# Performance work log

Hardware: AMD Instinct MI355X
Metric: run time of the kernel (lower is better)

## Reference

```python
import jax, jax.numpy as jnp
import numpy as np

B, L, TQ, D, H, S = 4, 64, 8, 768, 12, 2000
E = D // H
EPS = 1e-5


def _ln(x, g, b):
    m = jnp.mean(x, axis=-1, keepdims=True)
    v = jnp.mean(jnp.square(x - m), axis=-1, keepdims=True)
    return (x - m) * jax.lax.rsqrt(v + EPS) * g + b


def setup_inputs() -> dict:
    key = jax.random.key(0)
    ks = jax.random.split(key, 8)
    w = 0.02
    return {
        "target_tokens": jax.random.normal(ks[0], (B, L, TQ, D), jnp.float32),
        "key_bank": jax.random.normal(ks[1], (S, D), jnp.float32),
        "value_bank": jax.random.normal(ks[2], (S, D), jnp.float32),
        "bank_mask": jnp.ones((S,), jnp.int32),
        "Wq": jax.random.normal(ks[3], (D, D), jnp.float32) * w,
        "bq": jnp.zeros((D,), jnp.float32),
        "Wk": jax.random.normal(ks[4], (D, D), jnp.float32) * w,
        "bk": jnp.zeros((D,), jnp.float32),
        "Wv": jax.random.normal(ks[5], (D, D), jnp.float32) * w,
        "bv": jnp.zeros((D,), jnp.float32),
        "Wo": jax.random.normal(ks[6], (D, D), jnp.float32) * w,
        "bo": jnp.zeros((D,), jnp.float32),
        "g_q": jnp.ones((D,), jnp.float32),
        "beta_q": jnp.zeros((D,), jnp.float32),
        "g_kv": jnp.ones((D,), jnp.float32),
        "beta_kv": jnp.zeros((D,), jnp.float32),
    }


def reference(target_tokens, key_bank, value_bank, bank_mask,
              Wq, bq, Wk, bk, Wv, bv, Wo, bo,
              g_q, beta_q, g_kv, beta_kv):
    scale = 1.0 / np.sqrt(E)
    # LayerNorms
    Q_in = _ln(target_tokens, g_q, beta_q)            # (B,L,Tq,D)
    K_in = _ln(key_bank, g_kv, beta_kv)               # (S,D)
    V_in = _ln(value_bank, g_kv, beta_kv)             # (S,D)
    # Projections (torch Linear: x @ W.T + b)
    Q = (jnp.einsum('bltd,ed->blte', Q_in, Wq) + bq).reshape(B, L, TQ, H, E)
    K = (jnp.einsum('sd,ed->se', K_in, Wk) + bk).reshape(S, H, E)
    V = (jnp.einsum('sd,ed->se', V_in, Wv) + bv).reshape(S, H, E)
    # Scores over the bank (bank is shared across batch)
    scores = jnp.einsum('blthe,she->bhlts', Q, K) * scale  # (B,H,L,Tq,S)
    mask = bank_mask[None, None, None, None, :] != 0
    scores = jnp.where(mask, scores, -jnp.inf)
    A = jax.nn.softmax(scores, axis=-1)
    out = jnp.einsum('bhlts,she->blthe', A, V)             # (B,L,Tq,H,E)
    out_pooled = out.mean(axis=2).reshape(B, L, H * E)     # pool='mean' over Tq
    y = jnp.einsum('bld,ed->ble', out_pooled, Wo) + bo     # (B,L,D)
    return y
```

## Files before the change

### kernel.cpp

```cpp
#include <hip/hip_runtime.h>
#include <stdint.h>

typedef unsigned short u16;
typedef float f32x4 __attribute__((ext_vector_type(4)));
typedef __bf16 bf16x8 __attribute__((ext_vector_type(8)));

#define DDIM 768
#define NHEAD 12
#define EDIM 64
#define SREAL 2000
#define SPAD 2048
#define NQ 2048
#define NSPLIT 4

__device__ __forceinline__ u16 f2bf(float f) {
    unsigned u = __float_as_uint(f);
    return (u16)((u + 0x7fffu + ((u >> 16) & 1u)) >> 16);
}
__device__ __forceinline__ float bf2f(u16 v) {
    return __uint_as_float(((unsigned)v) << 16);
}

__device__ __forceinline__ void async16(const void* g, void* l) {
    __builtin_amdgcn_global_load_lds(
        (const __attribute__((address_space(1))) void*)(const void*)g,
        (__attribute__((address_space(3))) void*)l, 16, 0, 0);
}

__global__ __launch_bounds__(256) void prep_kernel(
    const float* __restrict__ Wq, const float* __restrict__ Wk, const float* __restrict__ Wv,
    const float* __restrict__ Wo,
    u16* __restrict__ Wqb, u16* __restrict__ Wkb, u16* __restrict__ Wvb, u16* __restrict__ Wob,
    const float* __restrict__ tgt, const float* __restrict__ keyb, const float* __restrict__ valb,
    const float* __restrict__ g_q, const float* __restrict__ b_q,
    const float* __restrict__ g_kv, const float* __restrict__ b_kv,
    u16* __restrict__ lnQ, u16* __restrict__ lnK, u16* __restrict__ lnV)
{
    int bx = blockIdx.x;
    if (bx < 2304) {
        int g = bx * 256 + threadIdx.x;
        const float* src; u16* dst; int idx; float sc = 1.f;
        if (g < 147456)      { src = Wq; dst = Wqb; idx = g; sc = 0.125f; }
        else if (g < 294912) { src = Wk; dst = Wkb; idx = g - 147456; }
        else if (g < 442368) { src = Wv; dst = Wvb; idx = g - 294912; }
        else                 { src = Wo; dst = Wob; idx = g - 442368; }
        f32x4 a = ((const f32x4*)src)[idx];
        ushort4 o;
        o.x = f2bf(a[0] * sc); o.y = f2bf(a[1] * sc);
        o.z = f2bf(a[2] * sc); o.w = f2bf(a[3] * sc);
        ((ushort4*)dst)[idx] = o;
        return;
    }
    int row = (bx - 2304) * 4 + (threadIdx.x >> 6);
    int l = threadIdx.x & 63;
    const float* src = nullptr; const float* gg; const float* bb; u16* dst;
    bool zero = false;
    if (row < 2048) {
        src = tgt + (size_t)row * DDIM; gg = g_q; bb = b_q; dst = lnQ + (size_t)row * DDIM;
    } else if (row < 4096) {
        int r = row - 2048; gg = g_kv; bb = b_kv; dst = lnK + (size_t)r * DDIM;
        if (r < SREAL) src = keyb + (size_t)r * DDIM; else zero = true;
    } else {
        int r = row - 4096; gg = g_kv; bb = b_kv; dst = lnV + (size_t)r * DDIM;
        if (r < SREAL) src = valb + (size_t)r * DDIM; else zero = true;
    }
    if (zero) {
        ushort4 z; z.x = 0; z.y = 0; z.z = 0; z.w = 0;
#pragma unroll
        for (int i = 0; i < 3; i++) ((ushort4*)dst)[l + 64 * i] = z;
        return;
    }
    f32x4 a[3];
#pragma unroll
    for (int i = 0; i < 3; i++) a[i] = ((const f32x4*)src)[l + 64 * i];
    float s = 0.f;
#pragma unroll
    for (int i = 0; i < 3; i++) { s += a[i][0] + a[i][1] + a[i][2] + a[i][3]; }
#pragma unroll
    for (int m = 1; m < 64; m <<= 1) s += __shfl_xor(s, m, 64);
    float mean = s * (1.f / 768.f);
    float v = 0.f;
#pragma unroll
    for (int i = 0; i < 3; i++)
#pragma unroll
        for (int j = 0; j < 4; j++) { float d = a[i][j] - mean; v += d * d; }
#pragma unroll
    for (int m = 1; m < 64; m <<= 1) v += __shfl_xor(v, m, 64);
    float rstd = rsqrtf(v * (1.f / 768.f) + 1e-5f);
#pragma unroll
    for (int i = 0; i < 3; i++) {
        f32x4 g4 = ((const f32x4*)gg)[l + 64 * i];
        f32x4 b4 = ((const f32x4*)bb)[l + 64 * i];
        ushort4 o;
        o.x = f2bf((a[i][0] - mean) * rstd * g4[0] + b4[0]);
        o.y = f2bf((a[i][1] - mean) * rstd * g4[1] + b4[1]);
        o.z = f2bf((a[i][2] - mean) * rstd * g4[2] + b4[2]);
        o.w = f2bf((a[i][3] - mean) * rstd * g4[3] + b4[3]);
        ((ushort4*)dst)[l + 64 * i] = o;
    }
}

__global__ __launch_bounds__(256) void proj_kernel(
    const u16* __restrict__ lnQ, const u16* __restrict__ lnK, const u16* __restrict__ lnV,
    const u16* __restrict__ Wqb, const u16* __restrict__ Wkb, const u16* __restrict__ Wvb,
    const float* __restrict__ bq, const float* __restrict__ bk, const float* __restrict__ bv,
    u16* __restrict__ Qm, u16* __restrict__ Km, u16* __restrict__ VmT)
{
    __shared__ u16 Ash[2][128 * 64];
    __shared__ u16 Bsh[2][64 * 64];
    const u16* A; const u16* W; const float* bias; float bscale; int z = blockIdx.z;
    if (z == 0)      { A = lnQ; W = Wqb; bias = bq; bscale = 0.125f; }
    else if (z == 1) { A = lnK; W = Wkb; bias = bk; bscale = 1.f; }
    else             { A = lnV; W = Wvb; bias = bv; bscale = 1.f; }
    int n0 = blockIdx.x * 64, m0 = blockIdx.y * 128;
    int t = threadIdx.x, l = t & 63, quad = l >> 4, c16 = l & 15;
    int w = t >> 6;

    f32x4 acc[2][4];
    f32x4 zz = {0.f, 0.f, 0.f, 0.f};
#pragma unroll
    for (int mi = 0; mi < 2; mi++)
#pragma unroll
        for (int ni = 0; ni < 4; ni++) acc[mi][ni] = zz;

#pragma unroll
    for (int i = 0; i < 4; i++) {
        int ch = i * 256 + t;
        int r = ch >> 3, pc = ch & 7, jc = pc ^ (r & 7);
        async16(A + (size_t)(m0 + r) * DDIM + jc * 8, (char*)Ash[0] + ch * 16);
    }
#pragma unroll
    for (int i = 0; i < 2; i++) {
        int ch = i * 256 + t;
        int r = ch >> 3, pc = ch & 7, jc = pc ^ (r & 7);
        async16(W + (size_t)(n0 + r) * DDIM + jc * 8, (char*)Bsh[0] + ch * 16);
    }
    for (int kt = 0; kt < 12; kt++) {
        int cur = kt & 1;
        __syncthreads();
        if (kt < 11) {
            int k0 = (kt + 1) * 64;
#pragma unroll
            for (int i = 0; i < 4; i++) {
                int ch = i * 256 + t;
                int r = ch >> 3, pc = ch & 7, jc = pc ^ (r & 7);
                async16(A + (size_t)(m0 + r) * DDIM + k0 + jc * 8, (char*)Ash[cur ^ 1] + ch * 16);
            }
#pragma unroll
            for (int i = 0; i < 2; i++) {
                int ch = i * 256 + t;
                int r = ch >> 3, pc = ch & 7, jc = pc ^ (r & 7);
                async16(W + (size_t)(n0 + r) * DDIM + k0 + jc * 8, (char*)Bsh[cur ^ 1] + ch * 16);
            }
        }
#pragma unroll
        for (int kk = 0; kk < 2; kk++) {
            bf16x8 a[2], b[4];
#pragma unroll
            for (int mi = 0; mi < 2; mi++) {
                int row = w * 32 + mi * 16 + c16;
                int p = (kk * 4 + quad) ^ (row & 7);
                a[mi] = *(const bf16x8*)(Ash[cur] + row * 64 + p * 8);
            }
#pragma unroll
            for (int ni = 0; ni < 4; ni++) {
                int row = ni * 16 + c16;
                int p = (kk * 4 + quad) ^ (row & 7);
                b[ni] = *(const bf16x8*)(Bsh[cur] + row * 64 + p * 8);
            }
#pragma unroll
            for (int mi = 0; mi < 2; mi++)
#pragma unroll
                for (int ni = 0; ni < 4; ni++)
                    acc[mi][ni] = __builtin_amdgcn_mfma_f32_16x16x32_bf16(a[mi], b[ni], acc[mi][ni], 0, 0, 0);
        }
        __syncthreads();
    }
    if (z < 2) {
        u16* out = (z == 0) ? Qm : Km;
        int Mact = (z == 0) ? NQ : SREAL;
#pragma unroll
        for (int mi = 0; mi < 2; mi++)
#pragma unroll
            for (int ni = 0; ni < 4; ni++) {
                int n = n0 + ni * 16 + c16;
                float bval = bias[n] * bscale;
#pragma unroll
                for (int r = 0; r < 4; r++) {
                    int m = m0 + w * 32 + mi * 16 + quad * 4 + r;
                    float val = (m < Mact) ? (acc[mi][ni][r] + bval) : 0.f;
                    out[(size_t)m * DDIM + n] = f2bf(val);
                }
            }
    } else {
#pragma unroll
        for (int mi = 0; mi < 2; mi++)
#pragma unroll
            for (int ni = 0; ni < 4; ni++) {
                int n = n0 + ni * 16 + c16;
                float bval = bias[n];
                int mbase = m0 + w * 32 + mi * 16 + quad * 4;
                ushort4 o;
                o.x = (mbase + 0 < SREAL) ? f2bf(acc[mi][ni][0] + bval) : (u16)0;
                o.y = (mbase + 1 < SREAL) ? f2bf(acc[mi][ni][1] + bval) : (u16)0;
                o.z = (mbase + 2 < SREAL) ? f2bf(acc[mi][ni][2] + bval) : (u16)0;
                o.w = (mbase + 3 < SREAL) ? f2bf(acc[mi][ni][3] + bval) : (u16)0;
                *(ushort4*)(VmT + (size_t)n * SPAD + mbase) = o;
            }
    }
}

__global__ __launch_bounds__(256, 4) void attn_kernel(
    const u16* __restrict__ Qm, const u16* __restrict__ Km, const u16* __restrict__ VmT,
    const int* __restrict__ bank_mask,
    u16* __restrict__ Opart, float* __restrict__ Lpart)
{
    __shared__ __align__(16) u16 SH[64 * 64 * 3];
    __shared__ float mk[64];
    u16* Ksh = SH;
    u16* Vsh = SH + 4096;
    u16* Psh = SH + 8192;
    int b = blockIdx.x;
    int xcd = b & 7, j = b >> 3;
    int grp = xcd * 6 + (j >> 5);
    int qt = j & 31;
    int sp = grp / NHEAD, h = grp - sp * NHEAD;
    int q0 = qt * 64;
    int t = threadIdx.x, w = t >> 6, l = t & 63, quad = l >> 4, c16 = l & 15;

    bf16x8 qf[2];
#pragma unroll
    for (int kk = 0; kk < 2; kk++) {
        int row = q0 + w * 16 + c16;
        qf[kk] = *(const bf16x8*)(Qm + (size_t)row * DDIM + h * EDIM + kk * 32 + quad * 8);
    }
    bf16x8 ones;
#pragma unroll
    for (int i = 0; i < 8; i++) ones[i] = (__bf16)1.0f;

    f32x4 zz = {0.f, 0.f, 0.f, 0.f};
    f32x4 of[4], ol;
#pragma unroll
    for (int nei = 0; nei < 4; nei++) of[nei] = zz;
    ol = zz;

    for (int sc = 0; sc < 8; sc++) {
        int s0 = sp * 512 + sc * 64;
#pragma unroll
        for (int i = 0; i < 2; i++) {
            int ch = i * 256 + t;
            int r = ch >> 3, pc = ch & 7, jc = pc ^ (r & 7);
            async16(Km + (size_t)(s0 + r) * DDIM + h * EDIM + jc * 8, (char*)Ksh + ch * 16);
        }
#pragma unroll
        for (int i = 0; i < 2; i++) {
            int ch = i * 256 + t;
            int e = ch >> 3, pc = ch & 7, jc = pc ^ (e & 7);
            async16(VmT + (size_t)(h * EDIM + e) * SPAD + s0 + jc * 8, (char*)Vsh + ch * 16);
        }
        if (t < 64) {
            int s = s0 + t;
            mk[t] = (s < SREAL && bank_mask[s] != 0) ? 1.f : 0.f;
        }
        __syncthreads();

        f32x4 sacc[4];
#pragma unroll
        for (int ni = 0; ni < 4; ni++) sacc[ni] = zz;
#pragma unroll
        for (int kk = 0; kk < 2; kk++) {
            bf16x8 kb[4];
#pragma unroll
            for (int ni = 0; ni < 4; ni++) {
                int row = ni * 16 + c16;
                int p = (kk * 4 + quad) ^ (row & 7);
                kb[ni] = *(const bf16x8*)(Ksh + row * 64 + p * 8);
            }
#pragma unroll
            for (int ni = 0; ni < 4; ni++)
                sacc[ni] = __builtin_amdgcn_mfma_f32_16x16x32_bf16(qf[kk], kb[ni], sacc[ni], 0, 0, 0);
        }
        float m01[4];
#pragma unroll
        for (int ni = 0; ni < 4; ni++) m01[ni] = mk[ni * 16 + c16];
#pragma unroll
        for (int ni = 0; ni < 4; ni++)
#pragma unroll
            for (int r = 0; r < 4; r++)
                sacc[ni][r] = __expf(sacc[ni][r]) * m01[ni];

#pragma unroll
        for (int ni = 0; ni < 4; ni++)
#pragma unroll
            for (int r = 0; r < 4; r++) {
                int row = w * 16 + quad * 4 + r;
                int col = ni * 16 + c16;
                int p = (col >> 3) ^ (row & 7);
                Psh[row * 64 + p * 8 + (col & 7)] = f2bf(sacc[ni][r]);
            }

#pragma unroll
        for (int kk = 0; kk < 2; kk++) {
            bf16x8 pa, vb[4];
            {
                int row = w * 16 + c16;
                int p = (kk * 4 + quad) ^ (row & 7);
                pa = *(const bf16x8*)(Psh + row * 64 + p * 8);
            }
#pragma unroll
            for (int nei = 0; nei < 4; nei++) {
                int e = nei * 16 + c16;
                int p = (kk * 4 + quad) ^ (e & 7);
                vb[nei] = *(const bf16x8*)(Vsh + e * 64 + p * 8);
            }
#pragma unroll
            for (int nei = 0; nei < 4; nei++)
                of[nei] = __builtin_amdgcn_mfma_f32_16x16x32_bf16(pa, vb[nei], of[nei], 0, 0, 0);
            ol = __builtin_amdgcn_mfma_f32_16x16x32_bf16(pa, ones, ol, 0, 0, 0);
        }
        __syncthreads();
    }

    float* Ost = (float*)SH + w * (16 * 68);
#pragma unroll
    for (int nei = 0; nei < 4; nei++)
#pragma unroll
        for (int r = 0; r < 4; r++)
            Ost[(quad * 4 + r) * 68 + nei * 16 + c16] = of[nei][r];
    int qq = l >> 2, cc = (l & 3) ^ (qq & 3);
    int base = grp * 32 + qt;
    uint4 packed[2];
    u16* pk = (u16*)packed;
#pragma unroll
    for (int jj = 0; jj < 4; jj++) {
        f32x4 v = *(const f32x4*)(Ost + qq * 68 + cc * 16 + jj * 4);
        pk[jj * 4 + 0] = f2bf(v[0]); pk[jj * 4 + 1] = f2bf(v[1]);
        pk[jj * 4 + 2] = f2bf(v[2]); pk[jj * 4 + 3] = f2bf(v[3]);
    }
    {
        u16* dst = Opart + (size_t)base * 4096 + (w * 16 + qq) * 64 + cc * 16;
        *(uint4*)dst = packed[0];
        *(uint4*)(dst + 8) = packed[1];
    }
    if (c16 == 0) {
#pragma unroll
        for (int r = 0; r < 4; r++) {
            int rin = w * 16 + quad * 4 + r;
            Lpart[(size_t)base * 64 + rin] = ol[r];
        }
    }
}

__global__ __launch_bounds__(256) void combine_kernel(
    const u16* __restrict__ Opart, const float* __restrict__ Lpart,
    u16* __restrict__ pooledb)
{
    int gi = blockIdx.x * 4 + (threadIdx.x >> 6);
    int e = threadIdx.x & 63;
    int lq = gi / NHEAD, h = gi - lq * NHEAD;
    float acc = 0.f;
#pragma unroll
    for (int row = 0; row < 8; row++) {
        int qrow = lq * 8 + row;
        int qt = qrow >> 6, rin = qrow & 63;
        float Ls = 0.f, val = 0.f;
#pragma unroll
        for (int sp = 0; sp < NSPLIT; sp++) {
            int base = (sp * NHEAD + h) * 32 + qt;
            Ls += Lpart[(size_t)base * 64 + rin];
            val += bf2f(Opart[(size_t)base * 4096 + rin * 64 + e]);
        }
        acc += val / Ls;
    }
    pooledb[(size_t)lq * DDIM + h * EDIM + e] = f2bf(acc * 0.125f);
}

__global__ __launch_bounds__(256) void wo_kernel(
    const u16* __restrict__ pb, const u16* __restrict__ Wob,
    const float* __restrict__ bo, float* __restrict__ y)
{
    __shared__ u16 Ash[64 * 128];
    __shared__ u16 Bsh[64 * 128];
    int m0 = blockIdx.x * 64, n0 = blockIdx.y * 64;
    int t = threadIdx.x, w = t >> 6, l = t & 63, quad = l >> 4, c16 = l & 15;

    f32x4 acc[4];
    f32x4 zz = {0.f, 0.f, 0.f, 0.f};
#pragma unroll
    for (int ni = 0; ni < 4; ni++) acc[ni] = zz;

    for (int kt = 0; kt < 6; kt++) {
        int k0 = kt * 128;
#pragma unroll
        for (int i = 0; i < 4; i++) {
            int ch = i * 256 + t;
            int r = ch >> 4, pc = ch & 15, jc = pc ^ (r & 15);
            async16(pb + (size_t)(m0 + r) * DDIM + k0 + jc * 8, (char*)Ash + ch * 16);
            async16(Wob + (size_t)(n0 + r) * DDIM + k0 + jc * 8, (char*)Bsh + ch * 16);
        }
        __syncthreads();
#pragma unroll
        for (int kk = 0; kk < 4; kk++) {
            int p = (kk * 4 + quad) ^ c16;
            bf16x8 a = *(const bf16x8*)(Ash + (w * 16 + c16) * 128 + p * 8);
            bf16x8 b[4];
#pragma unroll
            for (int ni = 0; ni < 4; ni++)
                b[ni] = *(const bf16x8*)(Bsh + (ni * 16 + c16) * 128 + p * 8);
#pragma unroll
            for (int ni = 0; ni < 4; ni++)
                acc[ni] = __builtin_amdgcn_mfma_f32_16x16x32_bf16(a, b[ni], acc[ni], 0, 0, 0);
        }
        __syncthreads();
    }
#pragma unroll
    for (int ni = 0; ni < 4; ni++) {
        int n = n0 + ni * 16 + c16;
        float bval = bo[n];
#pragma unroll
        for (int r = 0; r < 4; r++) {
            int m = m0 + w * 16 + quad * 4 + r;
            y[(size_t)m * DDIM + n] = acc[ni][r] + bval;
        }
    }
}

extern "C" void kernel_launch(void* const* d_in, const int* in_sizes, int n_in,
                              void* d_out, int out_size, void* d_ws, size_t ws_size,
                              hipStream_t stream)
{
    const float* tgt     = (const float*)d_in[0];
    const float* keyb    = (const float*)d_in[1];
    const float* valb    = (const float*)d_in[2];
    const int*   mask    = (const int*)d_in[3];
    const float* Wq      = (const float*)d_in[4];
    const float* bq      = (const float*)d_in[5];
    const float* Wk      = (const float*)d_in[6];
    const float* bk      = (const float*)d_in[7];
    const float* Wv      = (const float*)d_in[8];
    const float* bv      = (const float*)d_in[9];
    const float* Wo      = (const float*)d_in[10];
    const float* bo      = (const float*)d_in[11];
    const float* g_q     = (const float*)d_in[12];
    const float* beta_q  = (const float*)d_in[13];
    const float* g_kv    = (const float*)d_in[14];
    const float* beta_kv = (const float*)d_in[15];
    float* y = (float*)d_out;

    char* ws = (char*)d_ws;
    u16* Qm  = (u16*)(ws + 0);
    u16* Km  = (u16*)(ws + 3145728);
    u16* VmT = (u16*)(ws + 6291456);
    u16* Wob = (u16*)(ws + 9437184);
    u16* lnQ = (u16*)(ws + 10616832);
    u16* lnK = (u16*)(ws + 13762560);
    u16* lnV = (u16*)(ws + 16908288);
    u16* Wqb = (u16*)(ws + 20054016);
    u16* Wkb = (u16*)(ws + 21233664);
    u16* Wvb = (u16*)(ws + 22413312);
    u16*   Opart   = (u16*)(ws + 10616832);
    float* Lpart   = (float*)(ws + 23592960);
    u16*   pooledb = (u16*)(ws + 23986176);

    hipLaunchKernelGGL(prep_kernel, dim3(3840), dim3(256), 0, stream,
                       Wq, Wk, Wv, Wo, Wqb, Wkb, Wvb, Wob,
                       tgt, keyb, valb, g_q, beta_q, g_kv, beta_kv, lnQ, lnK, lnV);
    hipLaunchKernelGGL(proj_kernel, dim3(12, 16, 3), dim3(256), 0, stream,
                       lnQ, lnK, lnV, Wqb, Wkb, Wvb, bq, bk, bv, Qm, Km, VmT);
    hipLaunchKernelGGL(attn_kernel, dim3(1536), dim3(256), 0, stream,
                       Qm, Km, VmT, mask, Opart, Lpart);
    hipLaunchKernelGGL(combine_kernel, dim3(768), dim3(256), 0, stream,
                       Opart, Lpart, pooledb);
    hipLaunchKernelGGL(wo_kernel, dim3(4, 12), dim3(256), 0, stream,
                       pooledb, Wob, bo, y);
}
```

Before: 159.2 us.

## Fuse all stages into one persistent kernel with software grid barriers

Replaces the five separate launches (prep, projection, attention, combine, output projection) with a single persistent kernel of 512 blocks. The blocks loop over each stage's work units and synchronise through an atomic-counter grid barrier kept in the workspace, which is reset by a memset before each launch. The aim is to remove the launch gaps and tail effects between the small kernels. In exchange, attention occupancy drops from 4 to 2 blocks per CU under the new launch bounds, and there is a co-residency assumption plus a spin-timeout barrier that could break if not all 512 blocks are resident.

```diff
diff --git a/kernel.cpp b/kernel.cpp
--- a/kernel.cpp
+++ b/kernel.cpp
@@ -12,6 +12,8 @@
 #define SPAD 2048
 #define NQ 2048
 #define NSPLIT 4
+#define GRID 512
+#define BAR_OFF 25165824
 
 __device__ __forceinline__ u16 f2bf(float f) {
     unsigned u = __float_as_uint(f);
@@ -27,7 +29,28 @@
         (__attribute__((address_space(3))) void*)l, 16, 0, 0);
 }
 
-__global__ __launch_bounds__(256) void prep_kernel(
+__device__ __forceinline__ void grid_barrier(unsigned* bar) {
+    __syncthreads();
+    if (threadIdx.x == 0) {
+        __builtin_amdgcn_fence(__ATOMIC_SEQ_CST, "");
+        unsigned g = __hip_atomic_load(&bar[32], __ATOMIC_RELAXED, __HIP_MEMORY_SCOPE_SYSTEM);
+        unsigned a = __hip_atomic_fetch_add(&bar[0], 1u, __ATOMIC_ACQ_REL, __HIP_MEMORY_SCOPE_SYSTEM);
+        if (a == GRID - 1u) {
+            __hip_atomic_store(&bar[0], 0u, __ATOMIC_RELAXED, __HIP_MEMORY_SCOPE_SYSTEM);
+            __hip_atomic_fetch_add(&bar[32], 1u, __ATOMIC_RELEASE, __HIP_MEMORY_SCOPE_SYSTEM);
+        } else {
+            int tries = 1 << 20;
+            while (__hip_atomic_load(&bar[32], __ATOMIC_RELAXED, __HIP_MEMORY_SCOPE_SYSTEM) == g) {
+                __builtin_amdgcn_s_sleep(2);
+                if (--tries == 0) break;
+            }
+        }
+        __builtin_amdgcn_fence(__ATOMIC_SEQ_CST, "");
+    }
+    __syncthreads();
+}
+
+__device__ __forceinline__ void prep_unit(int bx, int t,
     const float* __restrict__ Wq, const float* __restrict__ Wk, const float* __restrict__ Wv,
     const float* __restrict__ Wo,
     u16* __restrict__ Wqb, u16* __restrict__ Wkb, u16* __restrict__ Wvb, u16* __restrict__ Wob,
@@ -36,9 +59,8 @@
     const float* __restrict__ g_kv, const float* __restrict__ b_kv,
     u16* __restrict__ lnQ, u16* __restrict__ lnK, u16* __restrict__ lnV)
 {
-    int bx = blockIdx.x;
     if (bx < 2304) {
-        int g = bx * 256 + threadIdx.x;
+        int g = bx * 256 + t;
         const float* src; u16* dst; int idx; float sc = 1.f;
         if (g < 147456)      { src = Wq; dst = Wqb; idx = g; sc = 0.125f; }
         else if (g < 294912) { src = Wk; dst = Wkb; idx = g - 147456; }
@@ -51,8 +73,8 @@
         ((ushort4*)dst)[idx] = o;
         return;
     }
-    int row = (bx - 2304) * 4 + (threadIdx.x >> 6);
-    int l = threadIdx.x & 63;
+    int row = (bx - 2304) * 4 + (t >> 6);
+    int l = t & 63;
     const float* src = nullptr; const float* gg; const float* bb; u16* dst;
     bool zero = false;
     if (row < 2048) {
@@ -100,20 +122,19 @@
     }
 }
 
-__global__ __launch_bounds__(256) void proj_kernel(
+__device__ __forceinline__ void proj_tile(int z, int m0, int n0, int t,
     const u16* __restrict__ lnQ, const u16* __restrict__ lnK, const u16* __restrict__ lnV,
     const u16* __restrict__ Wqb, const u16* __restrict__ Wkb, const u16* __restrict__ Wvb,
     const float* __restrict__ bq, const float* __restrict__ bk, const float* __restrict__ bv,
-    u16* __restrict__ Qm, u16* __restrict__ Km, u16* __restrict__ VmT)
+    u16* __restrict__ Qm, u16* __restrict__ Km, u16* __restrict__ VmT, char* SMEMC)
 {
-    __shared__ u16 Ash[2][128 * 64];
-    __shared__ u16 Bsh[2][64 * 64];
-    const u16* A; const u16* W; const float* bias; float bscale; int z = blockIdx.z;
+    u16* Ash0 = (u16*)SMEMC;
+    u16* Bsh0 = (u16*)(SMEMC + 32768);
+    const u16* A; const u16* W; const float* bias; float bscale;
     if (z == 0)      { A = lnQ; W = Wqb; bias = bq; bscale = 0.125f; }
     else if (z == 1) { A = lnK; W = Wkb; bias = bk; bscale = 1.f; }
     else             { A = lnV; W = Wvb; bias = bv; bscale = 1.f; }
-    int n0 = blockIdx.x * 64, m0 = blockIdx.y * 128;
-    int t = threadIdx.x, l = t & 63, quad = l >> 4, c16 = l & 15;
+    int l = t & 63, quad = l >> 4, c16 = l & 15;
     int w = t >> 6;
 
     f32x4 acc[2][4];
@@ -127,13 +148,13 @@
     for (int i = 0; i < 4; i++) {
         int ch = i * 256 + t;
         int r = ch >> 3, pc = ch & 7, jc = pc ^ (r & 7);
-        async16(A + (size_t)(m0 + r) * DDIM + jc * 8, (char*)Ash[0] + ch * 16);
+        async16(A + (size_t)(m0 + r) * DDIM + jc * 8, (char*)Ash0 + ch * 16);
     }
 #pragma unroll
     for (int i = 0; i < 2; i++) {
         int ch = i * 256 + t;
         int r = ch >> 3, pc = ch & 7, jc = pc ^ (r & 7);
-        async16(W + (size_t)(n0 + r) * DDIM + jc * 8, (char*)Bsh[0] + ch * 16);
+        async16(W + (size_t)(n0 + r) * DDIM + jc * 8, (char*)Bsh0 + ch * 16);
     }
     for (int kt = 0; kt < 12; kt++) {
         int cur = kt & 1;
@@ -144,13 +165,15 @@
             for (int i = 0; i < 4; i++) {
                 int ch = i * 256 + t;
                 int r = ch >> 3, pc = ch & 7, jc = pc ^ (r & 7);
-                async16(A + (size_t)(m0 + r) * DDIM + k0 + jc * 8, (char*)Ash[cur ^ 1] + ch * 16);
+                async16(A + (size_t)(m0 + r) * DDIM + k0 + jc * 8,
+                        (char*)(Ash0 + (cur ^ 1) * 8192) + ch * 16);
             }
 #pragma unroll
             for (int i = 0; i < 2; i++) {
                 int ch = i * 256 + t;
                 int r = ch >> 3, pc = ch & 7, jc = pc ^ (r & 7);
-                async16(W + (size_t)(n0 + r) * DDIM + k0 + jc * 8, (char*)Bsh[cur ^ 1] + ch * 16);
+                async16(W + (size_t)(n0 + r) * DDIM + k0 + jc * 8,
+                        (char*)(Bsh0 + (cur ^ 1) * 4096) + ch * 16);
             }
         }
 #pragma unroll
@@ -160,13 +183,13 @@
             for (int mi = 0; mi < 2; mi++) {
                 int row = w * 32 + mi * 16 + c16;
                 int p = (kk * 4 + quad) ^ (row & 7);
-                a[mi] = *(const bf16x8*)(Ash[cur] + row * 64 + p * 8);
+                a[mi] = *(const bf16x8*)(Ash0 + cur * 8192 + row * 64 + p * 8);
             }
 #pragma unroll
             for (int ni = 0; ni < 4; ni++) {
                 int row = ni * 16 + c16;
                 int p = (kk * 4 + quad) ^ (row & 7);
-                b[ni] = *(const bf16x8*)(Bsh[cur] + row * 64 + p * 8);
+                b[ni] = *(const bf16x8*)(Bsh0 + cur * 4096 + row * 64 + p * 8);
             }
 #pragma unroll
             for (int mi = 0; mi < 2; mi++)
@@ -210,23 +233,19 @@
     }
 }
 
-__global__ __launch_bounds__(256, 4) void attn_kernel(
+__device__ __forceinline__ void attn_tile(int grp, int qt, int t,
     const u16* __restrict__ Qm, const u16* __restrict__ Km, const u16* __restrict__ VmT,
     const int* __restrict__ bank_mask,
-    u16* __restrict__ Opart, float* __restrict__ Lpart)
+    u16* __restrict__ Opart, float* __restrict__ Lpart, char* SMEMC)
 {
-    __shared__ __align__(16) u16 SH[64 * 64 * 3];
-    __shared__ float mk[64];
+    u16* SH = (u16*)SMEMC;
+    float* mk = (float*)(SMEMC + 24576);
     u16* Ksh = SH;
     u16* Vsh = SH + 4096;
     u16* Psh = SH + 8192;
-    int b = blockIdx.x;
-    int xcd = b & 7, j = b >> 3;
-    int grp = xcd * 6 + (j >> 5);
-    int qt = j & 31;
     int sp = grp / NHEAD, h = grp - sp * NHEAD;
     int q0 = qt * 64;
-    int t = threadIdx.x, w = t >> 6, l = t & 63, quad = l >> 4, c16 = l & 15;
+    int w = t >> 6, l = t & 63, quad = l >> 4, c16 = l & 15;
 
     bf16x8 qf[2];
 #pragma unroll
@@ -349,40 +368,16 @@
             Lpart[(size_t)base * 64 + rin] = ol[r];
         }
     }
-}
-
-__global__ __launch_bounds__(256) void combine_kernel(
-    const u16* __restrict__ Opart, const float* __restrict__ Lpart,
-    u16* __restrict__ pooledb)
+    __syncthreads();
+}
+
+__device__ __forceinline__ void wo_tile(int m0, int n0, int t,
+    const u16* __restrict__ pb, const u16* __restrict__ Wob,
+    const float* __restrict__ bo, float* __restrict__ y, char* SMEMC)
 {
-    int gi = blockIdx.x * 4 + (threadIdx.x >> 6);
-    int e = threadIdx.x & 63;
-    int lq = gi / NHEAD, h = gi - lq * NHEAD;
-    float acc = 0.f;
-#pragma unroll
-    for (int row = 0; row < 8; row++) {
-        int qrow = lq * 8 + row;
-        int qt = qrow >> 6, rin = qrow & 63;
-        float Ls = 0.f, val = 0.f;
-#pragma unroll
-        for (int sp = 0; sp < NSPLIT; sp++) {
-            int base = (sp * NHEAD + h) * 32 + qt;
-            Ls += Lpart[(size_t)base * 64 + rin];
-            val += bf2f(Opart[(size_t)base * 4096 + rin * 64 + e]);
-        }
-        acc += val / Ls;
-    }
-    pooledb[(size_t)lq * DDIM + h * EDIM + e] = f2bf(acc * 0.125f);
-}
-
-__global__ __launch_bounds__(256) void wo_kernel(
-    const u16* __restrict__ pb, const u16* __restrict__ Wob,
-    const float* __restrict__ bo, float* __restrict__ y)
-{
-    __shared__ u16 Ash[64 * 128];
-    __shared__ u16 Bsh[64 * 128];
-    int m0 = blockIdx.x * 64, n0 = blockIdx.y * 64;
-    int t = threadIdx.x, w = t >> 6, l = t & 63, quad = l >> 4, c16 = l & 15;
+    u16* Ash = (u16*)SMEMC;
+    u16* Bsh = (u16*)(SMEMC + 16384);
+    int w = t >> 6, l = t & 63, quad = l >> 4, c16 = l & 15;
 
     f32x4 acc[4];
     f32x4 zz = {0.f, 0.f, 0.f, 0.f};
@@ -422,6 +417,89 @@
             int m = m0 + w * 16 + quad * 4 + r;
             y[(size_t)m * DDIM + n] = acc[ni][r] + bval;
         }
+    }
+}
+
+__global__ __launch_bounds__(256, 2) void mega_kernel(
+    const float* __restrict__ tgt, const float* __restrict__ keyb, const float* __restrict__ valb,
+    const int* __restrict__ bank_mask,
+    const float* __restrict__ Wq, const float* __restrict__ bq,
+    const float* __restrict__ Wk, const float* __restrict__ bk,
+    const float* __restrict__ Wv, const float* __restrict__ bv,
+    const float* __restrict__ Wo, const float* __restrict__ bo,
+    const float* __restrict__ g_q, const float* __restrict__ beta_q,
+    const float* __restrict__ g_kv, const float* __restrict__ beta_kv,
+    char* ws, float* y)
+{
+    __shared__ __align__(16) char SMEM[49152];
+    int bid = blockIdx.x, t = threadIdx.x;
+
+    u16* Qm  = (u16*)(ws + 0);
+    u16* Km  = (u16*)(ws + 3145728);
+    u16* VmT = (u16*)(ws + 6291456);
+    u16* Wob = (u16*)(ws + 9437184);
+    u16* lnQ = (u16*)(ws + 10616832);
+    u16* lnK = (u16*)(ws + 13762560);
+    u16* lnV = (u16*)(ws + 16908288);
+    u16* Wqb = (u16*)(ws + 20054016);
+    u16* Wkb = (u16*)(ws + 21233664);
+    u16* Wvb = (u16*)(ws + 22413312);
+    u16*   Opart   = (u16*)(ws + 10616832);
+    float* Lpart   = (float*)(ws + 23592960);
+    u16*   pooledb = (u16*)(ws + 23986176);
+    unsigned* bar  = (unsigned*)(ws + BAR_OFF);
+
+    for (int u = bid; u < 3840; u += GRID)
+        prep_unit(u, t, Wq, Wk, Wv, Wo, Wqb, Wkb, Wvb, Wob,
+                  tgt, keyb, valb, g_q, beta_q, g_kv, beta_kv, lnQ, lnK, lnV);
+    grid_barrier(bar);
+
+    for (int tl = bid; tl < 576; tl += GRID) {
+        int z = tl / 192, rem = tl - z * 192;
+        int m0 = (rem / 12) * 128;
+        int n0 = (rem - (rem / 12) * 12) * 64;
+        proj_tile(z, m0, n0, t, lnQ, lnK, lnV, Wqb, Wkb, Wvb, bq, bk, bv,
+                  Qm, Km, VmT, SMEM);
+        __syncthreads();
+    }
+    grid_barrier(bar);
+
+#pragma unroll
+    for (int it = 0; it < 3; it++) {
+        int T = bid + it * GRID;
+        int xcd = T & 7, j = T >> 3;
+        int grp = xcd * 6 + (j >> 5);
+        int qt = j & 31;
+        attn_tile(grp, qt, t, Qm, Km, VmT, bank_mask, Opart, Lpart, SMEM);
+    }
+    grid_barrier(bar);
+
+    for (int unit = bid; unit < 768; unit += GRID) {
+        int gi = unit * 4 + (t >> 6);
+        int e = t & 63;
+        int lq = gi / NHEAD, h = gi - lq * NHEAD;
+        float acc = 0.f;
+#pragma unroll
+        for (int row = 0; row < 8; row++) {
+            int qrow = lq * 8 + row;
+            int qt = qrow >> 6, rin = qrow & 63;
+            float Ls = 0.f, val = 0.f;
+#pragma unroll
+            for (int sp = 0; sp < NSPLIT; sp++) {
+                int base = (sp * NHEAD + h) * 32 + qt;
+                Ls += Lpart[(size_t)base * 64 + rin];
+                val += bf2f(Opart[(size_t)base * 4096 + rin * 64 + e]);
+            }
+            acc += val / Ls;
+        }
+        pooledb[(size_t)lq * DDIM + h * EDIM + e] = f2bf(acc * 0.125f);
+    }
+    grid_barrier(bar);
+
+    if (bid < 48) {
+        int m0 = (bid & 3) * 64;
+        int n0 = (bid >> 2) * 64;
+        wo_tile(m0, n0, t, pooledb, Wob, bo, y, SMEM);
     }
 }
 
@@ -446,31 +524,11 @@
     const float* g_kv    = (const float*)d_in[14];
     const float* beta_kv = (const float*)d_in[15];
     float* y = (float*)d_out;
-
     char* ws = (char*)d_ws;
-    u16* Qm  = (u16*)(ws + 0);
-    u16* Km  = (u16*)(ws + 3145728);
-    u16* VmT = (u16*)(ws + 6291456);
-    u16* Wob = (u16*)(ws + 9437184);
-    u16* lnQ = (u16*)(ws + 10616832);
-    u16* lnK = (u16*)(ws + 13762560);
-    u16* lnV = (u16*)(ws + 16908288);
-    u16* Wqb = (u16*)(ws + 20054016);
-    u16* Wkb = (u16*)(ws + 21233664);
-    u16* Wvb = (u16*)(ws + 22413312);
-    u16*   Opart   = (u16*)(ws + 10616832);
-    float* Lpart   = (float*)(ws + 23592960);
-    u16*   pooledb = (u16*)(ws + 23986176);
-
-    hipLaunchKernelGGL(prep_kernel, dim3(3840), dim3(256), 0, stream,
-                       Wq, Wk, Wv, Wo, Wqb, Wkb, Wvb, Wob,
-                       tgt, keyb, valb, g_q, beta_q, g_kv, beta_kv, lnQ, lnK, lnV);
-    hipLaunchKernelGGL(proj_kernel, dim3(12, 16, 3), dim3(256), 0, stream,
-                       lnQ, lnK, lnV, Wqb, Wkb, Wvb, bq, bk, bv, Qm, Km, VmT);
-    hipLaunchKernelGGL(attn_kernel, dim3(1536), dim3(256), 0, stream,
-                       Qm, Km, VmT, mask, Opart, Lpart);
-    hipLaunchKernelGGL(combine_kernel, dim3(768), dim3(256), 0, stream,
-                       Opart, Lpart, pooledb);
-    hipLaunchKernelGGL(wo_kernel, dim3(4, 12), dim3(256), 0, stream,
-                       pooledb, Wob, bo, y);
-}
+
+    hipMemsetAsync(ws + BAR_OFF, 0, 256, stream);
+
+    hipLaunchKernelGGL(mega_kernel, dim3(GRID), dim3(256), 0, stream,
+                       tgt, keyb, valb, mask, Wq, bq, Wk, bk, Wv, bv, Wo, bo,
+                       g_q, beta_q, g_kv, beta_kv, ws, y);
+}
```

Result: slower. 301.5 us (+89.3%).

## Double-buffer K/V tiles in attention and precompute bank mask bits in registers

Applied to the files above, without the earlier changes.

The attention kernel now keeps two K/V tile buffers in LDS and issues the async loads for the next 64-row bank chunk before computing on the current one. This overlaps global-to-LDS traffic with MFMA work and removes one barrier per iteration. The per-chunk mask load into shared memory is replaced by a 32-bit register bitmask built once at kernel start. A trailing __syncthreads in the projection GEMM loop is also dropped. The larger LDS footprint can lower occupancy, and dropping the GEMM barrier relies on its existing buffering to stay race-free.

```diff
diff --git a/kernel.cpp b/kernel.cpp
--- a/kernel.cpp
+++ b/kernel.cpp
@@ -174,7 +174,6 @@
                 for (int ni = 0; ni < 4; ni++)
                     acc[mi][ni] = __builtin_amdgcn_mfma_f32_16x16x32_bf16(a[mi], b[ni], acc[mi][ni], 0, 0, 0);
         }
-        __syncthreads();
     }
     if (z < 2) {
         u16* out = (z == 0) ? Qm : Km;
@@ -215,11 +214,8 @@
     const int* __restrict__ bank_mask,
     u16* __restrict__ Opart, float* __restrict__ Lpart)
 {
-    __shared__ __align__(16) u16 SH[64 * 64 * 3];
-    __shared__ float mk[64];
-    u16* Ksh = SH;
-    u16* Vsh = SH + 4096;
-    u16* Psh = SH + 8192;
+    __shared__ __align__(16) u16 SH[64 * 64 * 5];
+    u16* Psh = SH + 16384;
     int b = blockIdx.x;
     int xcd = b & 7, j = b >> 3;
     int grp = xcd * 6 + (j >> 5);
@@ -238,31 +234,59 @@
 #pragma unroll
     for (int i = 0; i < 8; i++) ones[i] = (__bf16)1.0f;
 
+    unsigned mbits = 0;
+#pragma unroll
+    for (int sc = 0; sc < 8; sc++)
+#pragma unroll
+        for (int ni = 0; ni < 4; ni++) {
+            int s = sp * 512 + sc * 64 + ni * 16 + c16;
+            int ok = (s < SREAL) ? bank_mask[s] : 0;
+            mbits |= (ok != 0 ? 1u : 0u) << (sc * 4 + ni);
+        }
+
     f32x4 zz = {0.f, 0.f, 0.f, 0.f};
     f32x4 of[4], ol;
 #pragma unroll
     for (int nei = 0; nei < 4; nei++) of[nei] = zz;
     ol = zz;
 
-    for (int sc = 0; sc < 8; sc++) {
-        int s0 = sp * 512 + sc * 64;
+    {
+        int s0 = sp * 512;
 #pragma unroll
         for (int i = 0; i < 2; i++) {
             int ch = i * 256 + t;
             int r = ch >> 3, pc = ch & 7, jc = pc ^ (r & 7);
-            async16(Km + (size_t)(s0 + r) * DDIM + h * EDIM + jc * 8, (char*)Ksh + ch * 16);
+            async16(Km + (size_t)(s0 + r) * DDIM + h * EDIM + jc * 8, (char*)SH + ch * 16);
         }
 #pragma unroll
         for (int i = 0; i < 2; i++) {
             int ch = i * 256 + t;
             int e = ch >> 3, pc = ch & 7, jc = pc ^ (e & 7);
-            async16(VmT + (size_t)(h * EDIM + e) * SPAD + s0 + jc * 8, (char*)Vsh + ch * 16);
-        }
-        if (t < 64) {
-            int s = s0 + t;
-            mk[t] = (s < SREAL && bank_mask[s] != 0) ? 1.f : 0.f;
-        }
+            async16(VmT + (size_t)(h * EDIM + e) * SPAD + s0 + jc * 8, (char*)(SH + 8192) + ch * 16);
+        }
+    }
+
+    for (int sc = 0; sc < 8; sc++) {
         __syncthreads();
+        if (sc < 7) {
+            int s0 = sp * 512 + (sc + 1) * 64;
+            u16* Kd = SH + ((sc + 1) & 1) * 4096;
+            u16* Vd = SH + 8192 + ((sc + 1) & 1) * 4096;
+#pragma unroll
+            for (int i = 0; i < 2; i++) {
+                int ch = i * 256 + t;
+                int r = ch >> 3, pc = ch & 7, jc = pc ^ (r & 7);
+                async16(Km + (size_t)(s0 + r) * DDIM + h * EDIM + jc * 8, (char*)Kd + ch * 16);
+            }
+#pragma unroll
+            for (int i = 0; i < 2; i++) {
+                int ch = i * 256 + t;
+                int e = ch >> 3, pc = ch & 7, jc = pc ^ (e & 7);
+                async16(VmT + (size_t)(h * EDIM + e) * SPAD + s0 + jc * 8, (char*)Vd + ch * 16);
+            }
+        }
+        const u16* Kc = SH + (sc & 1) * 4096;
+        const u16* Vc = SH + 8192 + (sc & 1) * 4096;
 
         f32x4 sacc[4];
 #pragma unroll
@@ -274,20 +298,19 @@
             for (int ni = 0; ni < 4; ni++) {
                 int row = ni * 16 + c16;
                 int p = (kk * 4 + quad) ^ (row & 7);
-                kb[ni] = *(const bf16x8*)(Ksh + row * 64 + p * 8);
+                kb[ni] = *(const bf16x8*)(Kc + row * 64 + p * 8);
             }
 #pragma unroll
             for (int ni = 0; ni < 4; ni++)
                 sacc[ni] = __builtin_amdgcn_mfma_f32_16x16x32_bf16(qf[kk], kb[ni], sacc[ni], 0, 0, 0);
         }
-        float m01[4];
-#pragma unroll
-        for (int ni = 0; ni < 4; ni++) m01[ni] = mk[ni * 16 + c16];
-#pragma unroll
-        for (int ni = 0; ni < 4; ni++)
+#pragma unroll
+        for (int ni = 0; ni < 4; ni++) {
+            float m01 = (float)((mbits >> (sc * 4 + ni)) & 1u);
 #pragma unroll
             for (int r = 0; r < 4; r++)
-                sacc[ni][r] = __expf(sacc[ni][r]) * m01[ni];
+                sacc[ni][r] = __expf(sacc[ni][r]) * m01;
+        }
 
 #pragma unroll
         for (int ni = 0; ni < 4; ni++)
@@ -311,15 +334,15 @@
             for (int nei = 0; nei < 4; nei++) {
                 int e = nei * 16 + c16;
                 int p = (kk * 4 + quad) ^ (e & 7);
-                vb[nei] = *(const bf16x8*)(Vsh + e * 64 + p * 8);
+                vb[nei] = *(const bf16x8*)(Vc + e * 64 + p * 8);
             }
 #pragma unroll
             for (int nei = 0; nei < 4; nei++)
                 of[nei] = __builtin_amdgcn_mfma_f32_16x16x32_bf16(pa, vb[nei], of[nei], 0, 0, 0);
             ol = __builtin_amdgcn_mfma_f32_16x16x32_bf16(pa, ones, ol, 0, 0, 0);
         }
-        __syncthreads();
-    }
+    }
+    __syncthreads();
 
     float* Ost = (float*)SH + w * (16 * 68);
 #pragma unroll
```

Measured after the change: 167.0 us. 1.05x slower.
